# Kernel optimization log

Measured on AMD Instinct MI355X. Metric: run time of the kernel, lower is better.

The kernel has to match this reference:

```python
import jax, jax.numpy as jnp
import numpy as np

DIM_EMB = 1024
NUM_HEADS = 16
DIM_HEAD = DIM_EMB // NUM_HEADS  # 64


def setup_inputs() -> dict:
    key = jax.random.key(0)
    k1, k2, k3 = jax.random.split(key, 3)
    x = jax.random.normal(k1, (4, 2048, DIM_EMB), dtype=jnp.float32)
    # nn.Linear(dim_embedding, 3*h*d, bias=False): weight shape [out, in]
    w_qkv = jax.random.normal(k2, (3 * NUM_HEADS * DIM_HEAD, DIM_EMB), dtype=jnp.float32) * (DIM_EMB ** -0.5)
    w_out = jax.random.normal(k3, (DIM_EMB, NUM_HEADS * DIM_HEAD), dtype=jnp.float32) * ((NUM_HEADS * DIM_HEAD) ** -0.5)
    return {"x": x, "w_qkv": w_qkv, "w_out": w_out}


def reference(x, w_qkv, w_out):
    b, t, _ = x.shape
    scale = DIM_HEAD ** -0.5
    qkv = jnp.einsum('bte,fe->btf', x, w_qkv)  # [b, t, 3*h*d]
    qkv = qkv.reshape(b, t, 3, NUM_HEADS, DIM_HEAD)  # fused dim order (k h d)
    q, k, v = qkv[:, :, 0], qkv[:, :, 1], qkv[:, :, 2]  # each [b, t, h, d]
    scores = jnp.einsum('bihd,bjhd->bhij', q, k) * scale  # [b, h, t, t]
    weights = jax.nn.softmax(scores, axis=-1)
    attn = jnp.einsum('bhij,bjhd->bhid', weights, v)  # [b, h, t, d]
    concat = attn.transpose(0, 2, 1, 3).reshape(b, t, NUM_HEADS * DIM_HEAD)
    return jnp.einsum('btf,ef->bte', concat, w_out)
```

## Files before the change

### kernel.cpp

```cpp
#include <hip/hip_runtime.h>

#define DI __device__ __forceinline__

typedef float  f32x2  __attribute__((ext_vector_type(2)));
typedef float  f32x4  __attribute__((ext_vector_type(4)));
typedef float  f32x16 __attribute__((ext_vector_type(16)));
typedef __bf16 bf16x8 __attribute__((ext_vector_type(8)));
typedef unsigned u32x2 __attribute__((ext_vector_type(2)));
typedef unsigned u32x4 __attribute__((ext_vector_type(4)));

static constexpr int TB   = 2048;
static constexpr int NTOK = 8192;
static constexpr int EMB  = 1024;
static constexpr int FQKV = 3072;

DI unsigned short f2bf(float f) {
  union { float f; unsigned u; } v; v.f = f;
  unsigned r = v.u + 0x7FFFu + ((v.u >> 16) & 1u);
  return (unsigned short)(r >> 16);
}

DI unsigned pack2bf(float a, float b) {
#if __has_builtin(__builtin_amdgcn_cvt_pk_bf16_f32)
  typedef __bf16 bf16x2 __attribute__((ext_vector_type(2)));
  bf16x2 r = __builtin_amdgcn_cvt_pk_bf16_f32(a, b);
  return __builtin_bit_cast(unsigned, r);
#else
  unsigned ua = __builtin_bit_cast(unsigned, a) + 0x8000u;
  unsigned ub = __builtin_bit_cast(unsigned, b) + 0x8000u;
  return __builtin_amdgcn_perm(ub, ua, 0x07060302u);
#endif
}

DI void plswap(unsigned& a, unsigned& b) {
#if __has_builtin(__builtin_amdgcn_permlane32_swap)
  u32x2 r = __builtin_amdgcn_permlane32_swap(a, b, false, false);
  a = r.x; b = r.y;
#else
  const bool hi = (threadIdx.x & 32) != 0;
  unsigned ax = (unsigned)__shfl_xor((int)a, 32);
  unsigned bx = (unsigned)__shfl_xor((int)b, 32);
  unsigned na = hi ? bx : a;
  unsigned nb = hi ? b : ax;
  a = na; b = nb;
#endif
}

DI bf16x8 frag4(unsigned a, unsigned b, unsigned c, unsigned d) {
  u32x4 u = {a, b, c, d};
  return __builtin_bit_cast(bf16x8, u);
}

DI void gload16(const void* g, void* l) {
  __builtin_amdgcn_global_load_lds(
      (__attribute__((address_space(1))) void*)(g),
      (__attribute__((address_space(3))) void*)(l), 16, 0, 0);
}

DI void syncdrain() {
  __builtin_amdgcn_s_waitcnt(0);
  __syncthreads();
}

__global__ __launch_bounds__(256)
void cvt_kernel(const float4* __restrict__ x, const float4* __restrict__ wq,
                const float4* __restrict__ wo,
                ushort4* __restrict__ xb, ushort4* __restrict__ wqb,
                ushort4* __restrict__ wob) {
  const int i  = blockIdx.x * 256 + threadIdx.x;
  const int nx = NTOK * EMB / 4;
  const int nq = FQKV * EMB / 4;
  float4 v; ushort4* dst;
  if (i < nx)           { v = x[i];           dst = xb  + i; }
  else if (i < nx + nq) { v = wq[i - nx];     dst = wqb + (i - nx); }
  else                  { v = wo[i - nx - nq]; dst = wob + (i - nx - nq); }
  ushort4 p;
  p.x = f2bf(v.x); p.y = f2bf(v.y); p.z = f2bf(v.z); p.w = f2bf(v.w);
  *dst = p;
}

__global__ __launch_bounds__(512, 2)
void gemm256(const unsigned short* __restrict__ A,
             const unsigned short* __restrict__ Bt,
             const int K,
             unsigned short* __restrict__ qk,
             unsigned short* __restrict__ vT) {
  __shared__ unsigned short sA[2][256 * 64];
  __shared__ unsigned short sB[2][256 * 64];
  const int tid  = threadIdx.x;
  const int w    = tid >> 6;
  const int l    = tid & 63;
  const int quad = l >> 4;
  const int lr   = l & 15;
  const int nwg  = gridDim.x * gridDim.y;
  const int orig = blockIdx.y * gridDim.x + blockIdx.x;
  const int swz  = (orig & 7) * (nwg >> 3) + (orig >> 3);
  const int n0   = (swz % gridDim.x) * 256;
  const int m0   = (swz / gridDim.x) * 256;
  const int wm   = (w >> 2) * 128;
  const int wn   = (w & 3) * 64;

  f32x4 acc[8][4];
#pragma unroll
  for (int i = 0; i < 8; ++i)
#pragma unroll
    for (int j = 0; j < 4; ++j) acc[i][j] = {0.f, 0.f, 0.f, 0.f};

  const int srow8 = l >> 3;
  const int gsw   = ((l & 7) ^ srow8) * 8;
  const unsigned short* gA0 = A  + (long)(m0 + w * 8 + srow8) * K + gsw;
  const unsigned short* gB0 = Bt + (long)(n0 + w * 8 + srow8) * K + gsw;

  const int NT = K >> 6;

#define STAGE256(buf, kk)                                                      \
  do {                                                                         \
    _Pragma("unroll")                                                          \
    for (int jj = 0; jj < 4; ++jj) {                                           \
      gload16(gA0 + (long)jj * 64 * K + (kk), &sA[buf][(jj * 64 + w * 8) * 64]);\
      gload16(gB0 + (long)jj * 64 * K + (kk), &sB[buf][(jj * 64 + w * 8) * 64]);\
    }                                                                          \
  } while (0)

  STAGE256(0, 0);
  syncdrain();

  for (int t = 0; t < NT; ++t) {
    const int cur = t & 1;
    if (t + 1 < NT) STAGE256(cur ^ 1, (t + 1) * 64);
    const unsigned short* aS = &sA[cur][0];
    const unsigned short* bS = &sB[cur][0];
#pragma unroll
    for (int ks = 0; ks < 2; ++ks) {
      bf16x8 bfr[4];
#pragma unroll
      for (int nf = 0; nf < 4; ++nf) {
        const int r = wn + nf * 16 + lr;
        bfr[nf] = *(const bf16x8*)(bS + r * 64 + ((ks * 4 + quad) ^ (r & 7)) * 8);
      }
#pragma unroll
      for (int m = 0; m < 8; ++m) {
        const int ra = wm + m * 16 + lr;
        const bf16x8 af = *(const bf16x8*)(aS + ra * 64 + ((ks * 4 + quad) ^ (ra & 7)) * 8);
#pragma unroll
        for (int nf = 0; nf < 4; ++nf)
          acc[m][nf] = __builtin_amdgcn_mfma_f32_16x16x32_bf16(af, bfr[nf],
                                                               acc[m][nf], 0, 0, 0);
      }
    }
    syncdrain();
  }
#undef STAGE256

  if (n0 < 2048) {
    const float qs = (n0 < 1024) ? 0.18033688011112042f : 1.0f;
#pragma unroll
    for (int m = 0; m < 8; ++m) {
      const int row = m0 + wm + m * 16 + quad * 4;
#pragma unroll
      for (int nf = 0; nf < 4; ++nf) {
        const int col = n0 + wn + nf * 16 + lr;
#pragma unroll
        for (int r = 0; r < 4; ++r)
          qk[(long)(row + r) * 2048 + col] = f2bf(acc[m][nf][r] * qs);
      }
    }
  } else {
#pragma unroll
    for (int m = 0; m < 8; ++m) {
      const int tok = m0 + wm + m * 16 + quad * 4;
      const int bb  = tok >> 11, tt = tok & 2047;
#pragma unroll
      for (int nf = 0; nf < 4; ++nf) {
        const int fv = n0 - 2048 + wn + nf * 16 + lr;
        ushort4 p;
        p.x = f2bf(acc[m][nf][0]); p.y = f2bf(acc[m][nf][1]);
        p.z = f2bf(acc[m][nf][2]); p.w = f2bf(acc[m][nf][3]);
        *(ushort4*)(vT + ((long)(bb * 1024 + fv)) * 2048 + tt) = p;
      }
    }
  }
}

template <int MODE>
__global__ __launch_bounds__(256)
void gemm_bt(const unsigned short* __restrict__ A,
             const unsigned short* __restrict__ Bt,
             const int K,
             unsigned short* __restrict__ qk,
             unsigned short* __restrict__ vT,
             float* __restrict__ outp) {
  __shared__ unsigned short sA[2][128 * 32];
  __shared__ unsigned short sB[2][128 * 32];
  const int tid  = threadIdx.x;
  const int w    = tid >> 6;
  const int l    = tid & 63;
  const int quad = l >> 4;
  const int lr   = l & 15;
  const int nwg  = gridDim.x * gridDim.y;
  const int orig = blockIdx.y * gridDim.x + blockIdx.x;
  const int swzb = (orig & 7) * (nwg >> 3) + (orig >> 3);
  const int n0   = (swzb % gridDim.x) * 128;
  const int m0   = (swzb / gridDim.x) * 128;
  const int wm   = (w >> 1) * 64;
  const int wn   = (w & 1) * 64;

  f32x4 acc[4][4];
#pragma unroll
  for (int i = 0; i < 4; ++i)
#pragma unroll
    for (int j = 0; j < 4; ++j) acc[i][j] = {0.f, 0.f, 0.f, 0.f};

  const int srow = l >> 2;
  const int sg   = (l & 3) ^ ((l >> 3) & 3);
  const unsigned short* gA = A  + (long)(m0 + w * 32 + srow) * K + sg * 8;
  const unsigned short* gB = Bt + (long)(n0 + w * 32 + srow) * K + sg * 8;
  const int lofs = w * 1024;
  const int swz  = (lr >> 1) & 3;
  const int NT   = K >> 5;

  gload16(gA,          &sA[0][lofs]);
  gload16(gA + 16 * K, &sA[0][lofs + 512]);
  gload16(gB,          &sB[0][lofs]);
  gload16(gB + 16 * K, &sB[0][lofs + 512]);
  syncdrain();

  for (int t = 0; t < NT; ++t) {
    const int cur = t & 1;
    if (t + 1 < NT) {
      const int k0 = (t + 1) * 32;
      gload16(gA + k0,          &sA[cur ^ 1][lofs]);
      gload16(gA + k0 + 16 * K, &sA[cur ^ 1][lofs + 512]);
      gload16(gB + k0,          &sB[cur ^ 1][lofs]);
      gload16(gB + k0 + 16 * K, &sB[cur ^ 1][lofs + 512]);
    }
    bf16x8 af[4], bfr[4];
#pragma unroll
    for (int rt = 0; rt < 4; ++rt)
      af[rt] = *(const bf16x8*)(&sA[cur][(wm + rt * 16 + lr) * 32 + (quad ^ swz) * 8]);
#pragma unroll
    for (int ct = 0; ct < 4; ++ct)
      bfr[ct] = *(const bf16x8*)(&sB[cur][(wn + ct * 16 + lr) * 32 + (quad ^ swz) * 8]);
#pragma unroll
    for (int rt = 0; rt < 4; ++rt)
#pragma unroll
      for (int ct = 0; ct < 4; ++ct)
        acc[rt][ct] = __builtin_amdgcn_mfma_f32_16x16x32_bf16(af[rt], bfr[ct],
                                                              acc[rt][ct], 0, 0, 0);
    syncdrain();
  }

  if (MODE == 0) {
    if (n0 < 2048) {
      const float qs = (n0 < 1024) ? 0.18033688011112042f : 1.0f;
#pragma unroll
      for (int rt = 0; rt < 4; ++rt) {
        const int row = m0 + wm + rt * 16 + quad * 4;
#pragma unroll
        for (int ct = 0; ct < 4; ++ct) {
          const int col = n0 + wn + ct * 16 + lr;
#pragma unroll
          for (int r = 0; r < 4; ++r)
            qk[(long)(row + r) * 2048 + col] = f2bf(acc[rt][ct][r] * qs);
        }
      }
    } else {
#pragma unroll
      for (int rt = 0; rt < 4; ++rt) {
        const int tok = m0 + wm + rt * 16 + quad * 4;
        const int bb  = tok >> 11, tt = tok & 2047;
#pragma unroll
        for (int ct = 0; ct < 4; ++ct) {
          const int fv = n0 - 2048 + wn + ct * 16 + lr;
          ushort4 p;
          p.x = f2bf(acc[rt][ct][0]); p.y = f2bf(acc[rt][ct][1]);
          p.z = f2bf(acc[rt][ct][2]); p.w = f2bf(acc[rt][ct][3]);
          *(ushort4*)(vT + ((long)(bb * 1024 + fv)) * 2048 + tt) = p;
        }
      }
    }
  } else {
#pragma unroll
    for (int rt = 0; rt < 4; ++rt) {
      const int row = m0 + wm + rt * 16 + quad * 4;
#pragma unroll
      for (int ct = 0; ct < 4; ++ct) {
        const int col = n0 + wn + ct * 16 + lr;
#pragma unroll
        for (int r = 0; r < 4; ++r)
          outp[(long)(row + r) * 1024 + col] = acc[rt][ct][r];
      }
    }
  }
}

__global__ __launch_bounds__(256, 4)
void attn_kernel(const unsigned short* __restrict__ qk,
                 const unsigned short* __restrict__ vT,
                 unsigned short* __restrict__ attnb) {
  __shared__ unsigned short sK[2][64 * 64];
  __shared__ unsigned short sV[2][64 * 64];
  const int tid = threadIdx.x;
  const int w   = tid >> 6;
  const int l   = tid & 63;
  const int l31 = l & 31;
  const int lh  = l >> 5;
  const int h8  = lh * 8;
  const int bh  = blockIdx.x;
  const int hh  = bh & 15;
  const long tokbase = (long)(bh >> 4) * TB;
  const int qbase = blockIdx.y * 128 + w * 32;

  bf16x8 qf[4];
  {
    const unsigned short* qptr = qk + (tokbase + qbase + l31) * 2048 + hh * 64 + h8;
#pragma unroll
    for (int s = 0; s < 4; ++s) qf[s] = *(const bf16x8*)(qptr + s * 16);
  }

  const int srow = l >> 3;
  const int g    = (l & 7) ^ srow;
  const unsigned short* kbase =
      qk + (tokbase + w * 16 + srow) * 2048 + 1024 + hh * 64 + g * 8;
  const unsigned short* vbase =
      vT + ((long)bh * 64 + w * 16 + srow) * 2048 + g * 8;

  f32x16 oacc[2] = {{}, {}};
  f32x2 lp2 = {0.f, 0.f};

  gload16(kbase,            &sK[0][(w * 16 + 0) * 64]);
  gload16(kbase + 8 * 2048, &sK[0][(w * 16 + 8) * 64]);
  gload16(vbase,            &sV[0][(w * 16 + 0) * 64]);
  gload16(vbase + 8 * 2048, &sV[0][(w * 16 + 8) * 64]);
  syncdrain();

  for (int t = 0; t < 32; ++t) {
    const int buf = t & 1;
    if (t + 1 < 32) {
      const int k0 = (t + 1) * 64;
      const int nb = buf ^ 1;
      gload16(kbase + (long)k0 * 2048,            &sK[nb][(w * 16 + 0) * 64]);
      gload16(kbase + (long)k0 * 2048 + 8 * 2048, &sK[nb][(w * 16 + 8) * 64]);
      gload16(vbase + k0,                         &sV[nb][(w * 16 + 0) * 64]);
      gload16(vbase + k0 + 8 * 2048,              &sV[nb][(w * 16 + 8) * 64]);
    }
    const unsigned short* bK = sK[buf];
    const unsigned short* bV = sV[buf];

#pragma unroll
    for (int G = 0; G < 2; ++G) {
      f32x16 sacc = {};
      __builtin_amdgcn_s_setprio(1);
#pragma unroll
      for (int s = 0; s < 4; ++s) {
        const int key = G * 32 + l31;
        const int p   = (s * 2 + lh) ^ (key & 7);
        const bf16x8 kf = *(const bf16x8*)(bK + key * 64 + p * 8);
        sacc = __builtin_amdgcn_mfma_f32_32x32x16_bf16(kf, qf[s], sacc, 0, 0, 0);
      }
      __builtin_amdgcn_s_setprio(0);
      float e[16];
#pragma unroll
      for (int i = 0; i < 16; ++i) e[i] = __builtin_amdgcn_exp2f(sacc[i]);
#pragma unroll
      for (int i = 0; i < 8; ++i) {
        f32x2 pr = {e[2 * i], e[2 * i + 1]};
        lp2 += pr;
      }
      unsigned d[8];
#pragma unroll
      for (int i = 0; i < 8; ++i) d[i] = pack2bf(e[2 * i], e[2 * i + 1]);
      plswap(d[0], d[2]); plswap(d[1], d[3]);
      plswap(d[4], d[6]); plswap(d[5], d[7]);
      bf16x8 pp[2];
      pp[0] = frag4(d[0], d[1], d[2], d[3]);
      pp[1] = frag4(d[4], d[5], d[6], d[7]);
      __builtin_amdgcn_s_setprio(1);
#pragma unroll
      for (int sub = 0; sub < 2; ++sub) {
        const int gt  = (G * 2 + sub) * 2 + lh;
        const int d0r = l31, d1r = 32 + l31;
        const bf16x8 vf0 = *(const bf16x8*)(bV + d0r * 64 + ((gt ^ (d0r & 7))) * 8);
        const bf16x8 vf1 = *(const bf16x8*)(bV + d1r * 64 + ((gt ^ (d1r & 7))) * 8);
        oacc[0] = __builtin_amdgcn_mfma_f32_32x32x16_bf16(pp[sub], vf0, oacc[0], 0, 0, 0);
        oacc[1] = __builtin_amdgcn_mfma_f32_32x32x16_bf16(pp[sub], vf1, oacc[1], 0, 0, 0);
      }
      __builtin_amdgcn_s_setprio(0);
    }
    syncdrain();
  }

  const float lp = lp2.x + lp2.y;
  const float fs = lp + __shfl_xor(lp, 32);
  const float rc = 1.0f / fs;
#pragma unroll
  for (int r = 0; r < 16; ++r) {
    const int row = (r & 3) + 8 * (r >> 2) + 4 * lh;
    const float sc = __shfl(rc, row);
    const long base = (tokbase + qbase + row) * 1024 + hh * 64;
    attnb[base + l31]      = f2bf(oacc[0][r] * sc);
    attnb[base + 32 + l31] = f2bf(oacc[1][r] * sc);
  }
}

extern "C" void kernel_launch(void* const* d_in, const int* in_sizes, int n_in,
                              void* d_out, int out_size, void* d_ws, size_t ws_size,
                              hipStream_t stream) {
  const float* x    = (const float*)d_in[0];
  const float* wqkv = (const float*)d_in[1];
  const float* wout = (const float*)d_in[2];
  float* outp = (float*)d_out;

  unsigned short* xb    = (unsigned short*)d_ws;
  unsigned short* wqkvb = xb    + (long)NTOK * EMB;
  unsigned short* woutb = wqkvb + (long)FQKV * EMB;
  unsigned short* qkb   = woutb + (long)EMB * EMB;
  unsigned short* vTb   = qkb   + (long)NTOK * 2048;
  unsigned short* attnb = vTb   + (long)4 * 16 * 64 * TB;

  cvt_kernel<<<12288, 256, 0, stream>>>(
      (const float4*)x, (const float4*)wqkv, (const float4*)wout,
      (ushort4*)xb, (ushort4*)wqkvb, (ushort4*)woutb);

  gemm256<<<dim3(12, 32), 512, 0, stream>>>(xb, wqkvb, EMB, qkb, vTb);

  attn_kernel<<<dim3(64, 16), 256, 0, stream>>>(qkb, vTb, attnb);

  gemm_bt<1><<<dim3(8, 64), 256, 0, stream>>>(attnb, woutb, EMB, nullptr, nullptr, outp);
}
```

Measured before the change: 276.5 us.

## Replace full drain barriers with partial vmcnt waits in all GEMM and attention loops

Replaces the waitcnt(0)+__syncthreads drain at the end of each k-step with a partial vmcnt wait placed after the next stage's global-to-LDS loads are issued. The next tile's prefetch can then stay in flight while the current tile is consumed, instead of draining all loads every iteration. It also wraps the MFMA blocks in s_setprio and removes the unused MODE template from the output GEMM. Correctness now relies on vmcnt counts matching the exact number of issued loads and on the raw s_barrier ordering LDS reads before the buffer is overwritten.

```diff
diff --git a/kernel.cpp b/kernel.cpp
--- a/kernel.cpp
+++ b/kernel.cpp
@@ -57,10 +57,11 @@
       (__attribute__((address_space(3))) void*)(l), 16, 0, 0);
 }
 
-DI void syncdrain() {
-  __builtin_amdgcn_s_waitcnt(0);
-  __syncthreads();
-}
+DI void wait_vm8() { asm volatile("s_waitcnt vmcnt(8)" ::: "memory"); }
+DI void wait_vm4() { asm volatile("s_waitcnt vmcnt(4)" ::: "memory"); }
+DI void wait_vm0() { asm volatile("s_waitcnt vmcnt(0)" ::: "memory"); }
+DI void rbar()     { __builtin_amdgcn_s_barrier(); }
+DI void sfence()   { __builtin_amdgcn_sched_barrier(0); }
 
 __global__ __launch_bounds__(256)
 void cvt_kernel(const float4* __restrict__ x, const float4* __restrict__ wq,
@@ -123,11 +124,14 @@
   } while (0)
 
   STAGE256(0, 0);
-  syncdrain();
 
   for (int t = 0; t < NT; ++t) {
     const int cur = t & 1;
-    if (t + 1 < NT) STAGE256(cur ^ 1, (t + 1) * 64);
+    if (t + 1 < NT) { STAGE256(cur ^ 1, (t + 1) * 64); wait_vm8(); }
+    else            { wait_vm0(); }
+    sfence();
+    rbar();
+    sfence();
     const unsigned short* aS = &sA[cur][0];
     const unsigned short* bS = &sB[cur][0];
 #pragma unroll
@@ -138,6 +142,7 @@
         const int r = wn + nf * 16 + lr;
         bfr[nf] = *(const bf16x8*)(bS + r * 64 + ((ks * 4 + quad) ^ (r & 7)) * 8);
       }
+      __builtin_amdgcn_s_setprio(1);
 #pragma unroll
       for (int m = 0; m < 8; ++m) {
         const int ra = wm + m * 16 + lr;
@@ -147,8 +152,10 @@
           acc[m][nf] = __builtin_amdgcn_mfma_f32_16x16x32_bf16(af, bfr[nf],
                                                                acc[m][nf], 0, 0, 0);
       }
-    }
-    syncdrain();
+      __builtin_amdgcn_s_setprio(0);
+    }
+    sfence();
+    rbar();
   }
 #undef STAGE256
 
@@ -182,14 +189,11 @@
   }
 }
 
-template <int MODE>
 __global__ __launch_bounds__(256)
-void gemm_bt(const unsigned short* __restrict__ A,
-             const unsigned short* __restrict__ Bt,
-             const int K,
-             unsigned short* __restrict__ qk,
-             unsigned short* __restrict__ vT,
-             float* __restrict__ outp) {
+void gemm_out(const unsigned short* __restrict__ A,
+              const unsigned short* __restrict__ Bt,
+              const int K,
+              float* __restrict__ outp) {
   __shared__ unsigned short sA[2][128 * 32];
   __shared__ unsigned short sB[2][128 * 32];
   const int tid  = threadIdx.x;
@@ -223,7 +227,6 @@
   gload16(gA + 16 * K, &sA[0][lofs + 512]);
   gload16(gB,          &sB[0][lofs]);
   gload16(gB + 16 * K, &sB[0][lofs + 512]);
-  syncdrain();
 
   for (int t = 0; t < NT; ++t) {
     const int cur = t & 1;
@@ -233,7 +236,13 @@
       gload16(gA + k0 + 16 * K, &sA[cur ^ 1][lofs + 512]);
       gload16(gB + k0,          &sB[cur ^ 1][lofs]);
       gload16(gB + k0 + 16 * K, &sB[cur ^ 1][lofs + 512]);
-    }
+      wait_vm4();
+    } else {
+      wait_vm0();
+    }
+    sfence();
+    rbar();
+    sfence();
     bf16x8 af[4], bfr[4];
 #pragma unroll
     for (int rt = 0; rt < 4; ++rt)
@@ -241,55 +250,27 @@
 #pragma unroll
     for (int ct = 0; ct < 4; ++ct)
       bfr[ct] = *(const bf16x8*)(&sB[cur][(wn + ct * 16 + lr) * 32 + (quad ^ swz) * 8]);
+    __builtin_amdgcn_s_setprio(1);
 #pragma unroll
     for (int rt = 0; rt < 4; ++rt)
 #pragma unroll
       for (int ct = 0; ct < 4; ++ct)
         acc[rt][ct] = __builtin_amdgcn_mfma_f32_16x16x32_bf16(af[rt], bfr[ct],
                                                               acc[rt][ct], 0, 0, 0);
-    syncdrain();
-  }
-
-  if (MODE == 0) {
-    if (n0 < 2048) {
-      const float qs = (n0 < 1024) ? 0.18033688011112042f : 1.0f;
-#pragma unroll
-      for (int rt = 0; rt < 4; ++rt) {
-        const int row = m0 + wm + rt * 16 + quad * 4;
-#pragma unroll
-        for (int ct = 0; ct < 4; ++ct) {
-          const int col = n0 + wn + ct * 16 + lr;
-#pragma unroll
-          for (int r = 0; r < 4; ++r)
-            qk[(long)(row + r) * 2048 + col] = f2bf(acc[rt][ct][r] * qs);
-        }
-      }
-    } else {
-#pragma unroll
-      for (int rt = 0; rt < 4; ++rt) {
-        const int tok = m0 + wm + rt * 16 + quad * 4;
-        const int bb  = tok >> 11, tt = tok & 2047;
-#pragma unroll
-        for (int ct = 0; ct < 4; ++ct) {
-          const int fv = n0 - 2048 + wn + ct * 16 + lr;
-          ushort4 p;
-          p.x = f2bf(acc[rt][ct][0]); p.y = f2bf(acc[rt][ct][1]);
-          p.z = f2bf(acc[rt][ct][2]); p.w = f2bf(acc[rt][ct][3]);
-          *(ushort4*)(vT + ((long)(bb * 1024 + fv)) * 2048 + tt) = p;
-        }
-      }
-    }
-  } else {
-#pragma unroll
-    for (int rt = 0; rt < 4; ++rt) {
-      const int row = m0 + wm + rt * 16 + quad * 4;
-#pragma unroll
-      for (int ct = 0; ct < 4; ++ct) {
-        const int col = n0 + wn + ct * 16 + lr;
-#pragma unroll
-        for (int r = 0; r < 4; ++r)
-          outp[(long)(row + r) * 1024 + col] = acc[rt][ct][r];
-      }
+    __builtin_amdgcn_s_setprio(0);
+    sfence();
+    rbar();
+  }
+
+#pragma unroll
+  for (int rt = 0; rt < 4; ++rt) {
+    const int row = m0 + wm + rt * 16 + quad * 4;
+#pragma unroll
+    for (int ct = 0; ct < 4; ++ct) {
+      const int col = n0 + wn + ct * 16 + lr;
+#pragma unroll
+      for (int r = 0; r < 4; ++r)
+        outp[(long)(row + r) * 1024 + col] = acc[rt][ct][r];
     }
   }
 }
@@ -332,7 +313,6 @@
   gload16(kbase + 8 * 2048, &sK[0][(w * 16 + 8) * 64]);
   gload16(vbase,            &sV[0][(w * 16 + 0) * 64]);
   gload16(vbase + 8 * 2048, &sV[0][(w * 16 + 8) * 64]);
-  syncdrain();
 
   for (int t = 0; t < 32; ++t) {
     const int buf = t & 1;
@@ -343,7 +323,13 @@
       gload16(kbase + (long)k0 * 2048 + 8 * 2048, &sK[nb][(w * 16 + 8) * 64]);
       gload16(vbase + k0,                         &sV[nb][(w * 16 + 0) * 64]);
       gload16(vbase + k0 + 8 * 2048,              &sV[nb][(w * 16 + 8) * 64]);
-    }
+      wait_vm4();
+    } else {
+      wait_vm0();
+    }
+    sfence();
+    rbar();
+    sfence();
     const unsigned short* bK = sK[buf];
     const unsigned short* bV = sV[buf];
 
@@ -387,7 +373,8 @@
       }
       __builtin_amdgcn_s_setprio(0);
     }
-    syncdrain();
+    sfence();
+    rbar();
   }
 
   const float lp = lp2.x + lp2.y;
@@ -426,5 +413,5 @@
 
   attn_kernel<<<dim3(64, 16), 256, 0, stream>>>(qkb, vTb, attnb);
 
-  gemm_bt<1><<<dim3(8, 64), 256, 0, stream>>>(attnb, woutb, EMB, nullptr, nullptr, outp);
-}
+  gemm_out<<<dim3(8, 64), 256, 0, stream>>>(attnb, woutb, EMB, outp);
+}
```

After: 277.1 us. Within noise of the previous version (+0.2%).
